# Performance work log

Hardware: AMD Instinct MI355X
Metric: run time of the kernel (lower is better)

The kernel has to match this reference:

```python
import jax, jax.numpy as jnp
import numpy as np

B = 2048
VOCABS = [100000, 50000, 10, 3, 100, 50, 1000, 24, 5]  # user,item,age,gender,city,category,brand,hour,device
E = 16
EMB_DIMS = [E, E, E // 2, E // 4, E // 2, E // 2, E // 2, E // 4, E // 4]
NUM_FEATURES = sum(VOCABS) + 1  # +1 for the price column
DEEP_IN = sum(EMB_DIMS) + 1  # 77
HIDDEN = [256, 128, 64]


def setup_inputs() -> dict:
    key = jax.random.key(0)
    ks = iter(jax.random.split(key, 40))
    inp = {}
    names = ['user_id', 'item_id', 'age', 'gender', 'city', 'category', 'brand', 'hour', 'device']
    for name, v in zip(names, VOCABS):
        inp[name] = jax.random.randint(next(ks), (B, 1), 0, v, dtype=jnp.int32).astype(jnp.int64)
    inp['price'] = jax.random.uniform(next(ks), (B, 1), dtype=jnp.float32) * 100.0
    # embedding tables
    tab_names = ['emb_user', 'emb_item', 'emb_age', 'emb_gender', 'emb_city', 'emb_category', 'emb_brand', 'emb_hour', 'emb_device']
    for name, v, d in zip(tab_names, VOCABS, EMB_DIMS):
        inp[name] = jax.random.normal(next(ks), (v, d), dtype=jnp.float32) * 0.05
    # dense (1st-order) weights
    inp['w_dense'] = jax.random.normal(next(ks), (NUM_FEATURES,), dtype=jnp.float32) * 0.01
    inp['b_dense'] = jnp.zeros((), dtype=jnp.float32)
    # FM 2nd-order factors
    inp['fm_v'] = jax.random.normal(next(ks), (NUM_FEATURES, E), dtype=jnp.float32) * 0.01
    # deep MLP
    dims = [DEEP_IN] + HIDDEN
    for i in range(len(HIDDEN)):
        inp[f'W{i+1}'] = jax.random.normal(next(ks), (dims[i], dims[i + 1]), dtype=jnp.float32) * (1.0 / np.sqrt(dims[i]))
        inp[f'b{i+1}'] = jnp.zeros((dims[i + 1],), dtype=jnp.float32)
    inp['Wo'] = jax.random.normal(next(ks), (HIDDEN[-1], 1), dtype=jnp.float32) * (1.0 / np.sqrt(HIDDEN[-1]))
    inp['bo'] = jnp.zeros((1,), dtype=jnp.float32)
    return inp


def reference(user_id, item_id, age, gender, city, category, brand, price, hour, device,
              emb_user, emb_item, emb_age, emb_gender, emb_city, emb_category, emb_brand,
              emb_hour, emb_device, w_dense, b_dense, fm_v, W1, b1, W2, b2, W3, b3, Wo, bo):
    b = user_id.shape[0]
    rows = jnp.arange(b)
    ids = [user_id, item_id, age, gender, city, category, brand, hour, device]
    # one-hot style feature vector: (b, NUM_FEATURES)
    feat = jnp.zeros((b, NUM_FEATURES), dtype=price.dtype)
    off = 0
    for idx, v in zip(ids, VOCABS):
        feat = feat.at[rows, off + idx[:, 0]].set(1.0)
        off += v
    feat = feat.at[:, NUM_FEATURES - 1].set(price[:, 0] / 1000.0)

    # 1st-order linear part
    logit_dense = feat @ w_dense + b_dense  # (b,)

    # FM 2nd-order: 0.5 * sum_k [ (x@V)^2 - x^2 @ V^2 ]
    square_of_sum = jnp.square(feat @ fm_v)            # (b, E)
    sum_of_square = jnp.square(feat) @ jnp.square(fm_v)  # (b, E)
    logit_fm = 0.5 * jnp.sum(square_of_sum - sum_of_square, axis=1)  # (b,)

    # deep part: embedding lookups + MLP (dropout inactive / eval mode)
    tables = [emb_user, emb_item, emb_age, emb_gender, emb_city, emb_category, emb_brand, emb_hour, emb_device]
    embs = [t[i[:, 0]] for t, i in zip(tables, ids)]
    deep_in = jnp.concatenate(embs + [price], axis=1)  # (b, 77)
    h = jax.nn.relu(deep_in @ W1 + b1)
    h = jax.nn.relu(h @ W2 + b2)
    h = jax.nn.relu(h @ W3 + b3)
    logit_deep = (h @ Wo + bo)[:, 0]

    return logit_dense + logit_fm + logit_deep
```

## Files before the change

### kernel.cpp

```cpp
#include <hip/hip_runtime.h>


#define RPB 4
#define BATCH 2048
#define NF 151193

#define OFF0 0
#define OFF1 100000
#define OFF2 150000
#define OFF3 150010
#define OFF4 150013
#define OFF5 150113
#define OFF6 150163
#define OFF7 151163
#define OFF8 151187

typedef float f4 __attribute__((ext_vector_type(4)));

__device__ inline f4 relu4(f4 v) {
    f4 r;
    r.x = fmaxf(v.x, 0.0f); r.y = fmaxf(v.y, 0.0f);
    r.z = fmaxf(v.z, 0.0f); r.w = fmaxf(v.w, 0.0f);
    return r;
}

__global__ __launch_bounds__(256, 2) void deepfm_fused(
    const int* __restrict__ f_user, const int* __restrict__ f_item,
    const int* __restrict__ f_age, const int* __restrict__ f_gender,
    const int* __restrict__ f_city, const int* __restrict__ f_cat,
    const int* __restrict__ f_brand, const int* __restrict__ f_hour,
    const int* __restrict__ f_dev, const float* __restrict__ price,
    const float* __restrict__ e_user, const float* __restrict__ e_item,
    const float* __restrict__ e_age, const float* __restrict__ e_gender,
    const float* __restrict__ e_city, const float* __restrict__ e_cat,
    const float* __restrict__ e_brand, const float* __restrict__ e_hour,
    const float* __restrict__ e_dev,
    const float* __restrict__ w_dense, const float* __restrict__ b_dense,
    const float* __restrict__ fm_v,
    const float* __restrict__ W1, const float* __restrict__ b1,
    const float* __restrict__ W2, const float* __restrict__ b2,
    const float* __restrict__ W3, const float* __restrict__ b3,
    const float* __restrict__ Wo, const float* __restrict__ bo,
    float* __restrict__ out)
{
    __shared__ __align__(16) float x[RPB][80];
    __shared__ __align__(16) float h1s[RPB][256];
    __shared__ __align__(16) float h2s[RPB][128];
    __shared__ __align__(16) float pred[4096];
    __shared__ float row_extra[RPB];

    const int tid  = threadIdx.x;
    const int base = blockIdx.x * RPB;

    const f4* W1v = (const f4*)W1;
    const int kg1 = tid >> 6, ct1 = tid & 63;
    f4 w1r[20];
    {
        const int i0 = 20 * kg1;
        #pragma unroll
        for (int d = 0; d < 20; ++d) {
            const int i = i0 + d;
            w1r[d] = (i < 77) ? W1v[i * 64 + ct1] : (f4)0.0f;
        }
    }
    const f4 b1v  = ((const f4*)b1)[tid & 63];
    const f4 b2v  = ((const f4*)b2)[tid & 31];
    const f4 b3v  = ((const f4*)b3)[tid & 15];
    const f4 wo_r = ((const f4*)Wo)[tid & 15];
    const float bo_s = bo[0];

    if (tid < 128) {
        const int r = tid >> 5, l = tid & 31;
        const int gr = base + r;
        if (l < 16) x[r][ 0 + l] = e_user  [f_user[gr]   * 16 + l];
        if (l < 16) x[r][16 + l] = e_item  [f_item[gr]   * 16 + l];
        if (l <  8) x[r][32 + l] = e_age   [f_age[gr]    *  8 + l];
        if (l <  4) x[r][40 + l] = e_gender[f_gender[gr] *  4 + l];
        if (l <  8) x[r][44 + l] = e_city  [f_city[gr]   *  8 + l];
        if (l <  8) x[r][52 + l] = e_cat   [f_cat[gr]    *  8 + l];
        if (l <  8) x[r][60 + l] = e_brand [f_brand[gr]  *  8 + l];
        if (l <  4) x[r][68 + l] = e_hour  [f_hour[gr]   *  4 + l];
        if (l <  4) x[r][72 + l] = e_dev   [f_dev[gr]    *  4 + l];
        if (l == 0) x[r][76]     = price[gr];
        if (l == 1) x[r][77] = 0.0f;
        if (l == 2) x[r][78] = 0.0f;
        if (l == 3) x[r][79] = 0.0f;
    } else if (tid < 192) {
        const int r = (tid >> 4) & 3, k = tid & 15;
        const int gr = base + r;
        const int i0 = f_user[gr], i1 = f_item[gr], i2 = f_age[gr];
        const int i3 = f_gender[gr], i4 = f_city[gr], i5 = f_cat[gr];
        const int i6 = f_brand[gr], i7 = f_hour[gr], i8 = f_dev[gr];
        const float px = price[gr] * (1.0f / 1000.0f);
        float v, s, ssq;
        v = fm_v[(NF - 1) * 16 + k];
        s = px * v; ssq = s * s;
        v = fm_v[(OFF0 + i0) * 16 + k]; s += v; ssq += v * v;
        v = fm_v[(OFF1 + i1) * 16 + k]; s += v; ssq += v * v;
        v = fm_v[(OFF2 + i2) * 16 + k]; s += v; ssq += v * v;
        v = fm_v[(OFF3 + i3) * 16 + k]; s += v; ssq += v * v;
        v = fm_v[(OFF4 + i4) * 16 + k]; s += v; ssq += v * v;
        v = fm_v[(OFF5 + i5) * 16 + k]; s += v; ssq += v * v;
        v = fm_v[(OFF6 + i6) * 16 + k]; s += v; ssq += v * v;
        v = fm_v[(OFF7 + i7) * 16 + k]; s += v; ssq += v * v;
        v = fm_v[(OFF8 + i8) * 16 + k]; s += v; ssq += v * v;
        float q = 0.5f * (s * s - ssq);
        if (k == 0) {
            float d = b_dense[0] + px * w_dense[NF - 1];
            d += w_dense[OFF0 + i0];
            d += w_dense[OFF1 + i1];
            d += w_dense[OFF2 + i2];
            d += w_dense[OFF3 + i3];
            d += w_dense[OFF4 + i4];
            d += w_dense[OFF5 + i5];
            d += w_dense[OFF6 + i6];
            d += w_dense[OFF7 + i7];
            d += w_dense[OFF8 + i8];
            q += d;
        }
        q += __shfl_xor(q, 8);
        q += __shfl_xor(q, 4);
        q += __shfl_xor(q, 2);
        q += __shfl_xor(q, 1);
        if (k == 0) row_extra[r] = q;
    }
    __syncthreads();

    const f4* hv1 = (const f4*)h1s;
    const f4* hv2 = (const f4*)h2s;
    f4* pv = (f4*)pred;
    f4 w2r[32];
    {
        const f4* xv = (const f4*)x;
        f4 acc0 = 0, acc1 = 0, acc2 = 0, acc3 = 0;
        #pragma unroll
        for (int c = 0; c < 5; ++c) {
            const int q = 5 * kg1 + c;
            f4 xa0 = xv[ 0 + q];
            f4 xa1 = xv[20 + q];
            f4 xa2 = xv[40 + q];
            f4 xa3 = xv[60 + q];
            acc0 += xa0.x * w1r[4*c] + xa0.y * w1r[4*c+1] + xa0.z * w1r[4*c+2] + xa0.w * w1r[4*c+3];
            acc1 += xa1.x * w1r[4*c] + xa1.y * w1r[4*c+1] + xa1.z * w1r[4*c+2] + xa1.w * w1r[4*c+3];
            acc2 += xa2.x * w1r[4*c] + xa2.y * w1r[4*c+1] + xa2.z * w1r[4*c+2] + xa2.w * w1r[4*c+3];
            acc3 += xa3.x * w1r[4*c] + xa3.y * w1r[4*c+1] + xa3.z * w1r[4*c+2] + xa3.w * w1r[4*c+3];
        }
        {
            const int kg = tid >> 5, ct = tid & 31;
            const f4* W2v = (const f4*)W2;
            const int i0 = 32 * kg;
            #pragma unroll
            for (int d = 0; d < 32; ++d) w2r[d] = W2v[(i0 + d) * 32 + ct];
        }
        pv[(kg1 * 4 + 0) * 64 + ct1] = acc0;
        pv[(kg1 * 4 + 1) * 64 + ct1] = acc1;
        pv[(kg1 * 4 + 2) * 64 + ct1] = acc2;
        pv[(kg1 * 4 + 3) * 64 + ct1] = acc3;
    }
    __syncthreads();
    {
        const int r = tid >> 6, c4 = tid & 63;
        f4 s = pv[(0 + r) * 64 + c4] + pv[(4 + r) * 64 + c4]
             + pv[(8 + r) * 64 + c4] + pv[(12 + r) * 64 + c4];
        s += b1v;
        ((f4*)h1s)[r * 64 + c4] = relu4(s);
    }
    __syncthreads();

    f4 w3r[8];
    {
        const int kg = tid >> 5, ct = tid & 31;
        f4 acc0 = 0, acc1 = 0, acc2 = 0, acc3 = 0;
        #pragma unroll
        for (int c = 0; c < 8; ++c) {
            const int q = 8 * kg + c;
            f4 xa0 = hv1[  0 + q];
            f4 xa1 = hv1[ 64 + q];
            f4 xa2 = hv1[128 + q];
            f4 xa3 = hv1[192 + q];
            acc0 += xa0.x * w2r[4*c] + xa0.y * w2r[4*c+1] + xa0.z * w2r[4*c+2] + xa0.w * w2r[4*c+3];
            acc1 += xa1.x * w2r[4*c] + xa1.y * w2r[4*c+1] + xa1.z * w2r[4*c+2] + xa1.w * w2r[4*c+3];
            acc2 += xa2.x * w2r[4*c] + xa2.y * w2r[4*c+1] + xa2.z * w2r[4*c+2] + xa2.w * w2r[4*c+3];
            acc3 += xa3.x * w2r[4*c] + xa3.y * w2r[4*c+1] + xa3.z * w2r[4*c+2] + xa3.w * w2r[4*c+3];
        }
        {
            const int kg3 = tid >> 4, ct3 = tid & 15;
            const f4* W3v = (const f4*)W3;
            const int i0 = 8 * kg3;
            #pragma unroll
            for (int d = 0; d < 8; ++d) w3r[d] = W3v[(i0 + d) * 16 + ct3];
        }
        pv[(kg * 4 + 0) * 32 + ct] = acc0;
        pv[(kg * 4 + 1) * 32 + ct] = acc1;
        pv[(kg * 4 + 2) * 32 + ct] = acc2;
        pv[(kg * 4 + 3) * 32 + ct] = acc3;
    }
    __syncthreads();
    if (tid < 128) {
        const int r = tid >> 5, c4 = tid & 31;
        f4 s = 0;
        #pragma unroll
        for (int kg = 0; kg < 8; ++kg) s += pv[(kg * 4 + r) * 32 + c4];
        s += b2v;
        ((f4*)h2s)[r * 32 + c4] = relu4(s);
    }
    __syncthreads();

    {
        const int kg = tid >> 4, ct = tid & 15;
        f4 acc0 = 0, acc1 = 0, acc2 = 0, acc3 = 0;
        #pragma unroll
        for (int c = 0; c < 2; ++c) {
            const int q = 2 * kg + c;
            f4 xa0 = hv2[ 0 + q];
            f4 xa1 = hv2[32 + q];
            f4 xa2 = hv2[64 + q];
            f4 xa3 = hv2[96 + q];
            acc0 += xa0.x * w3r[4*c] + xa0.y * w3r[4*c+1] + xa0.z * w3r[4*c+2] + xa0.w * w3r[4*c+3];
            acc1 += xa1.x * w3r[4*c] + xa1.y * w3r[4*c+1] + xa1.z * w3r[4*c+2] + xa1.w * w3r[4*c+3];
            acc2 += xa2.x * w3r[4*c] + xa2.y * w3r[4*c+1] + xa2.z * w3r[4*c+2] + xa2.w * w3r[4*c+3];
            acc3 += xa3.x * w3r[4*c] + xa3.y * w3r[4*c+1] + xa3.z * w3r[4*c+2] + xa3.w * w3r[4*c+3];
        }
        pv[(kg * 4 + 0) * 16 + ct] = acc0;
        pv[(kg * 4 + 1) * 16 + ct] = acc1;
        pv[(kg * 4 + 2) * 16 + ct] = acc2;
        pv[(kg * 4 + 3) * 16 + ct] = acc3;
    }
    __syncthreads();

    if (tid < 64) {
        const int r = tid >> 4, c4 = tid & 15;
        f4 s = 0;
        #pragma unroll
        for (int kg = 0; kg < 16; ++kg) s += pv[(kg * 4 + r) * 16 + c4];
        s += b3v;
        f4 h = relu4(s);
        float t = h.x * wo_r.x + h.y * wo_r.y + h.z * wo_r.z + h.w * wo_r.w;
        t += __shfl_xor(t, 8);
        t += __shfl_xor(t, 4);
        t += __shfl_xor(t, 2);
        t += __shfl_xor(t, 1);
        if (c4 == 0) out[base + r] = t + bo_s + row_extra[r];
    }
}

extern "C" void kernel_launch(void* const* d_in, const int* in_sizes, int n_in,
                              void* d_out, int out_size, void* d_ws, size_t ws_size,
                              hipStream_t stream) {
    const int*   f_user   = (const int*)  d_in[0];
    const int*   f_item   = (const int*)  d_in[1];
    const int*   f_age    = (const int*)  d_in[2];
    const int*   f_gender = (const int*)  d_in[3];
    const int*   f_city   = (const int*)  d_in[4];
    const int*   f_cat    = (const int*)  d_in[5];
    const int*   f_brand  = (const int*)  d_in[6];
    const int*   f_hour   = (const int*)  d_in[7];
    const int*   f_dev    = (const int*)  d_in[8];
    const float* price    = (const float*)d_in[9];
    const float* e_user   = (const float*)d_in[10];
    const float* e_item   = (const float*)d_in[11];
    const float* e_age    = (const float*)d_in[12];
    const float* e_gender = (const float*)d_in[13];
    const float* e_city   = (const float*)d_in[14];
    const float* e_cat    = (const float*)d_in[15];
    const float* e_brand  = (const float*)d_in[16];
    const float* e_hour   = (const float*)d_in[17];
    const float* e_dev    = (const float*)d_in[18];
    const float* w_dense  = (const float*)d_in[19];
    const float* b_dense  = (const float*)d_in[20];
    const float* fm_v     = (const float*)d_in[21];
    const float* W1       = (const float*)d_in[22];
    const float* b1       = (const float*)d_in[23];
    const float* W2       = (const float*)d_in[24];
    const float* b2       = (const float*)d_in[25];
    const float* W3       = (const float*)d_in[26];
    const float* b3       = (const float*)d_in[27];
    const float* Wo       = (const float*)d_in[28];
    const float* bo       = (const float*)d_in[29];
    float* out = (float*)d_out;

    dim3 grid(BATCH / RPB);
    dim3 block(256);
    deepfm_fused<<<grid, block, 0, stream>>>(
        f_user, f_item, f_age, f_gender, f_city, f_cat, f_brand, f_hour, f_dev,
        price, e_user, e_item, e_age, e_gender, e_city, e_cat, e_brand, e_hour,
        e_dev, w_dense, b_dense, fm_v, W1, b1, W2, b2, W3, b3, Wo, bo, out);
}
```

Before: 133.2 us.

## Double block to 512 threads and stream MLP weights instead of register prefetch

Raises the block size from 256 to 512 threads and splits each MLP layer's K dimension across twice as many thread groups. Weights are now loaded from global memory right where they are used, replacing the earlier register prefetch of W1/W2/W3. The partial-sum reductions now cover more groups. The intent is to cut per-thread register pressure and latency with more parallelism, at the cost of extra LDS reduction traffic and weight loads that are no longer overlapped with the previous layer.

```diff
diff --git a/kernel.cpp b/kernel.cpp
--- a/kernel.cpp
+++ b/kernel.cpp
@@ -24,7 +24,7 @@
     return r;
 }
 
-__global__ __launch_bounds__(256, 2) void deepfm_fused(
+__global__ __launch_bounds__(512, 4) void deepfm_fused(
     const int* __restrict__ f_user, const int* __restrict__ f_item,
     const int* __restrict__ f_age, const int* __restrict__ f_gender,
     const int* __restrict__ f_city, const int* __restrict__ f_cat,
@@ -43,26 +43,15 @@
     const float* __restrict__ Wo, const float* __restrict__ bo,
     float* __restrict__ out)
 {
-    __shared__ __align__(16) float x[RPB][80];
+    __shared__ __align__(16) float x[RPB][96];
     __shared__ __align__(16) float h1s[RPB][256];
     __shared__ __align__(16) float h2s[RPB][128];
-    __shared__ __align__(16) float pred[4096];
+    __shared__ __align__(16) float pred[8192];
     __shared__ float row_extra[RPB];
 
     const int tid  = threadIdx.x;
     const int base = blockIdx.x * RPB;
 
-    const f4* W1v = (const f4*)W1;
-    const int kg1 = tid >> 6, ct1 = tid & 63;
-    f4 w1r[20];
-    {
-        const int i0 = 20 * kg1;
-        #pragma unroll
-        for (int d = 0; d < 20; ++d) {
-            const int i = i0 + d;
-            w1r[d] = (i < 77) ? W1v[i * 64 + ct1] : (f4)0.0f;
-        }
-    }
     const f4 b1v  = ((const f4*)b1)[tid & 63];
     const f4 b2v  = ((const f4*)b2)[tid & 31];
     const f4 b3v  = ((const f4*)b3)[tid & 15];
@@ -82,9 +71,7 @@
         if (l <  4) x[r][68 + l] = e_hour  [f_hour[gr]   *  4 + l];
         if (l <  4) x[r][72 + l] = e_dev   [f_dev[gr]    *  4 + l];
         if (l == 0) x[r][76]     = price[gr];
-        if (l == 1) x[r][77] = 0.0f;
-        if (l == 2) x[r][78] = 0.0f;
-        if (l == 3) x[r][79] = 0.0f;
+        if (l >= 13) x[r][64 + l] = 0.0f;
     } else if (tid < 192) {
         const int r = (tid >> 4) & 3, k = tid & 15;
         const int gr = base + r;
@@ -129,66 +116,63 @@
     const f4* hv1 = (const f4*)h1s;
     const f4* hv2 = (const f4*)h2s;
     f4* pv = (f4*)pred;
-    f4 w2r[32];
+
     {
-        const f4* xv = (const f4*)x;
+        const int kg = tid >> 6, ct = tid & 63;
+        const f4* W1v = (const f4*)W1;
+        const f4* xv  = (const f4*)x;
         f4 acc0 = 0, acc1 = 0, acc2 = 0, acc3 = 0;
         #pragma unroll
-        for (int c = 0; c < 5; ++c) {
-            const int q = 5 * kg1 + c;
+        for (int c = 0; c < 3; ++c) {
+            const int i = 12 * kg + 4 * c, q = 3 * kg + c;
             f4 xa0 = xv[ 0 + q];
-            f4 xa1 = xv[20 + q];
-            f4 xa2 = xv[40 + q];
-            f4 xa3 = xv[60 + q];
-            acc0 += xa0.x * w1r[4*c] + xa0.y * w1r[4*c+1] + xa0.z * w1r[4*c+2] + xa0.w * w1r[4*c+3];
-            acc1 += xa1.x * w1r[4*c] + xa1.y * w1r[4*c+1] + xa1.z * w1r[4*c+2] + xa1.w * w1r[4*c+3];
-            acc2 += xa2.x * w1r[4*c] + xa2.y * w1r[4*c+1] + xa2.z * w1r[4*c+2] + xa2.w * w1r[4*c+3];
-            acc3 += xa3.x * w1r[4*c] + xa3.y * w1r[4*c+1] + xa3.z * w1r[4*c+2] + xa3.w * w1r[4*c+3];
-        }
-        {
-            const int kg = tid >> 5, ct = tid & 31;
-            const f4* W2v = (const f4*)W2;
-            const int i0 = 32 * kg;
-            #pragma unroll
-            for (int d = 0; d < 32; ++d) w2r[d] = W2v[(i0 + d) * 32 + ct];
-        }
-        pv[(kg1 * 4 + 0) * 64 + ct1] = acc0;
-        pv[(kg1 * 4 + 1) * 64 + ct1] = acc1;
-        pv[(kg1 * 4 + 2) * 64 + ct1] = acc2;
-        pv[(kg1 * 4 + 3) * 64 + ct1] = acc3;
-    }
-    __syncthreads();
-    {
+            f4 xa1 = xv[24 + q];
+            f4 xa2 = xv[48 + q];
+            f4 xa3 = xv[72 + q];
+            f4 w0 = (i + 0 < 77) ? W1v[(i + 0) * 64 + ct] : (f4)0.0f;
+            f4 w1 = (i + 1 < 77) ? W1v[(i + 1) * 64 + ct] : (f4)0.0f;
+            f4 w2 = (i + 2 < 77) ? W1v[(i + 2) * 64 + ct] : (f4)0.0f;
+            f4 w3 = (i + 3 < 77) ? W1v[(i + 3) * 64 + ct] : (f4)0.0f;
+            acc0 += xa0.x * w0 + xa0.y * w1 + xa0.z * w2 + xa0.w * w3;
+            acc1 += xa1.x * w0 + xa1.y * w1 + xa1.z * w2 + xa1.w * w3;
+            acc2 += xa2.x * w0 + xa2.y * w1 + xa2.z * w2 + xa2.w * w3;
+            acc3 += xa3.x * w0 + xa3.y * w1 + xa3.z * w2 + xa3.w * w3;
+        }
+        pv[(kg * 4 + 0) * 64 + ct] = acc0;
+        pv[(kg * 4 + 1) * 64 + ct] = acc1;
+        pv[(kg * 4 + 2) * 64 + ct] = acc2;
+        pv[(kg * 4 + 3) * 64 + ct] = acc3;
+    }
+    __syncthreads();
+    if (tid < 256) {
         const int r = tid >> 6, c4 = tid & 63;
-        f4 s = pv[(0 + r) * 64 + c4] + pv[(4 + r) * 64 + c4]
-             + pv[(8 + r) * 64 + c4] + pv[(12 + r) * 64 + c4];
+        f4 s = 0;
+        #pragma unroll
+        for (int kg = 0; kg < 8; ++kg) s += pv[(kg * 4 + r) * 64 + c4];
         s += b1v;
         ((f4*)h1s)[r * 64 + c4] = relu4(s);
     }
     __syncthreads();
 
-    f4 w3r[8];
     {
         const int kg = tid >> 5, ct = tid & 31;
+        const f4* W2v = (const f4*)W2;
         f4 acc0 = 0, acc1 = 0, acc2 = 0, acc3 = 0;
         #pragma unroll
-        for (int c = 0; c < 8; ++c) {
-            const int q = 8 * kg + c;
+        for (int c = 0; c < 4; ++c) {
+            const int q = 4 * kg + c;
             f4 xa0 = hv1[  0 + q];
             f4 xa1 = hv1[ 64 + q];
             f4 xa2 = hv1[128 + q];
             f4 xa3 = hv1[192 + q];
-            acc0 += xa0.x * w2r[4*c] + xa0.y * w2r[4*c+1] + xa0.z * w2r[4*c+2] + xa0.w * w2r[4*c+3];
-            acc1 += xa1.x * w2r[4*c] + xa1.y * w2r[4*c+1] + xa1.z * w2r[4*c+2] + xa1.w * w2r[4*c+3];
-            acc2 += xa2.x * w2r[4*c] + xa2.y * w2r[4*c+1] + xa2.z * w2r[4*c+2] + xa2.w * w2r[4*c+3];
-            acc3 += xa3.x * w2r[4*c] + xa3.y * w2r[4*c+1] + xa3.z * w2r[4*c+2] + xa3.w * w2r[4*c+3];
-        }
-        {
-            const int kg3 = tid >> 4, ct3 = tid & 15;
-            const f4* W3v = (const f4*)W3;
-            const int i0 = 8 * kg3;
-            #pragma unroll
-            for (int d = 0; d < 8; ++d) w3r[d] = W3v[(i0 + d) * 16 + ct3];
+            f4 w0 = W2v[(4 * q + 0) * 32 + ct];
+            f4 w1 = W2v[(4 * q + 1) * 32 + ct];
+            f4 w2 = W2v[(4 * q + 2) * 32 + ct];
+            f4 w3 = W2v[(4 * q + 3) * 32 + ct];
+            acc0 += xa0.x * w0 + xa0.y * w1 + xa0.z * w2 + xa0.w * w3;
+            acc1 += xa1.x * w0 + xa1.y * w1 + xa1.z * w2 + xa1.w * w3;
+            acc2 += xa2.x * w0 + xa2.y * w1 + xa2.z * w2 + xa2.w * w3;
+            acc3 += xa3.x * w0 + xa3.y * w1 + xa3.z * w2 + xa3.w * w3;
         }
         pv[(kg * 4 + 0) * 32 + ct] = acc0;
         pv[(kg * 4 + 1) * 32 + ct] = acc1;
@@ -200,7 +184,7 @@
         const int r = tid >> 5, c4 = tid & 31;
         f4 s = 0;
         #pragma unroll
-        for (int kg = 0; kg < 8; ++kg) s += pv[(kg * 4 + r) * 32 + c4];
+        for (int kg = 0; kg < 16; ++kg) s += pv[(kg * 4 + r) * 32 + c4];
         s += b2v;
         ((f4*)h2s)[r * 32 + c4] = relu4(s);
     }
@@ -208,18 +192,22 @@
 
     {
         const int kg = tid >> 4, ct = tid & 15;
+        const f4* W3v = (const f4*)W3;
         f4 acc0 = 0, acc1 = 0, acc2 = 0, acc3 = 0;
-        #pragma unroll
-        for (int c = 0; c < 2; ++c) {
-            const int q = 2 * kg + c;
+        {
+            const int q = kg;
             f4 xa0 = hv2[ 0 + q];
             f4 xa1 = hv2[32 + q];
             f4 xa2 = hv2[64 + q];
             f4 xa3 = hv2[96 + q];
-            acc0 += xa0.x * w3r[4*c] + xa0.y * w3r[4*c+1] + xa0.z * w3r[4*c+2] + xa0.w * w3r[4*c+3];
-            acc1 += xa1.x * w3r[4*c] + xa1.y * w3r[4*c+1] + xa1.z * w3r[4*c+2] + xa1.w * w3r[4*c+3];
-            acc2 += xa2.x * w3r[4*c] + xa2.y * w3r[4*c+1] + xa2.z * w3r[4*c+2] + xa2.w * w3r[4*c+3];
-            acc3 += xa3.x * w3r[4*c] + xa3.y * w3r[4*c+1] + xa3.z * w3r[4*c+2] + xa3.w * w3r[4*c+3];
+            f4 w0 = W3v[(4 * q + 0) * 16 + ct];
+            f4 w1 = W3v[(4 * q + 1) * 16 + ct];
+            f4 w2 = W3v[(4 * q + 2) * 16 + ct];
+            f4 w3 = W3v[(4 * q + 3) * 16 + ct];
+            acc0 = xa0.x * w0 + xa0.y * w1 + xa0.z * w2 + xa0.w * w3;
+            acc1 = xa1.x * w0 + xa1.y * w1 + xa1.z * w2 + xa1.w * w3;
+            acc2 = xa2.x * w0 + xa2.y * w1 + xa2.z * w2 + xa2.w * w3;
+            acc3 = xa3.x * w0 + xa3.y * w1 + xa3.z * w2 + xa3.w * w3;
         }
         pv[(kg * 4 + 0) * 16 + ct] = acc0;
         pv[(kg * 4 + 1) * 16 + ct] = acc1;
@@ -232,7 +220,7 @@
         const int r = tid >> 4, c4 = tid & 15;
         f4 s = 0;
         #pragma unroll
-        for (int kg = 0; kg < 16; ++kg) s += pv[(kg * 4 + r) * 16 + c4];
+        for (int kg = 0; kg < 32; ++kg) s += pv[(kg * 4 + r) * 16 + c4];
         s += b3v;
         f4 h = relu4(s);
         float t = h.x * wo_r.x + h.y * wo_r.y + h.z * wo_r.z + h.w * wo_r.w;
@@ -280,7 +268,7 @@
     float* out = (float*)d_out;
 
     dim3 grid(BATCH / RPB);
-    dim3 block(256);
+    dim3 block(512);
     deepfm_fused<<<grid, block, 0, stream>>>(
         f_user, f_item, f_age, f_gender, f_city, f_cat, f_brand, f_hour, f_dev,
         price, e_user, e_item, e_age, e_gender, e_city, e_cat, e_brand, e_hour,
```

Result: no change. 134.0 us (+0.7%).
